# Performance work log

Measured on AMD Instinct MI355X. Metric: run time of the kernel, lower is better.

## Reference

```python
import jax, jax.numpy as jnp
import numpy as np

N = 2_000_000      # total active voxels across the batch (post sparse-conv stack)
C = 128            # channels out of the last SparseConv3d block
B = 256            # batch_size
NUM_CLASSES = 4


def _linear_params(key, fan_in, fan_out):
    kw, kb = jax.random.split(key)
    bound = 1.0 / np.sqrt(fan_in)
    W = jax.random.uniform(kw, (fan_in, fan_out), jnp.float32, -bound, bound)
    b = jax.random.uniform(kb, (fan_out,), jnp.float32, -bound, bound)
    return W, b


def setup_inputs() -> dict:
    key = jax.random.key(0)
    ks = jax.random.split(key, 6)
    features = jax.random.normal(ks[0], (N, C), dtype=jnp.float32)
    batch_ids = jnp.sort(jax.random.randint(ks[1], (N,), 0, B, dtype=jnp.int32))
    W1, b1 = _linear_params(ks[2], 2 * C, 128)
    W2, b2 = _linear_params(ks[3], 128, 64)
    W3, b3 = _linear_params(ks[4], 64, 32)
    W4, b4 = _linear_params(ks[5], 32, NUM_CLASSES)
    return {
        "features": features, "batch_ids": batch_ids, "batch_size": B,
        "W1": W1, "b1": b1, "W2": W2, "b2": b2,
        "W3": W3, "b3": b3, "W4": W4, "b4": b4,
    }


def reference(features, batch_ids, batch_size, W1, b1, W2, b2, W3, b3, W4, b4):
    # Fused segment mean+max pooling (replaces the per-batch Python loop).
    seg_sum = jax.ops.segment_sum(features, batch_ids, num_segments=batch_size,
                                  indices_are_sorted=True)            # [B, C]
    counts = jax.ops.segment_sum(jnp.ones((features.shape[0],), features.dtype),
                                 batch_ids, num_segments=batch_size,
                                 indices_are_sorted=True)             # [B]
    seg_max = jax.ops.segment_max(features, batch_ids, num_segments=batch_size,
                                  indices_are_sorted=True)            # [B, C]
    nonempty = (counts > 0)[:, None]
    seg_mean = jnp.where(nonempty, seg_sum / jnp.maximum(counts, 1.0)[:, None], 0.0)
    seg_max = jnp.where(nonempty, seg_max, 0.0)  # empty segments -> zeros (as in torch code)
    pooled = jnp.concatenate([seg_mean, seg_max], axis=1)             # [B, 2C]
    # fc head (Dropout is identity in eval mode)
    h = jax.nn.relu(pooled @ W1 + b1)
    h = jax.nn.relu(h @ W2 + b2)
    h = jax.nn.relu(h @ W3 + b3)
    return h @ W4 + b4                                                # [B, num_classes]
```

## Files before the change

### kernel.cpp

```cpp
#include <hip/hip_runtime.h>

#define CC 128
#define C4V 32
#define RPB 1024
#define UNR 8

typedef float f4v __attribute__((ext_vector_type(4)));

__device__ __forceinline__ f4v vsplat(float x) {
    f4v r; r.x = x; r.y = x; r.z = x; r.w = x; return r;
}

__device__ __forceinline__ unsigned fkey(float f) {
    unsigned b = __float_as_uint(f);
    return (b & 0x80000000u) ? ~b : (b | 0x80000000u);
}
__device__ __forceinline__ float fdec(unsigned k) {
    unsigned b = (k & 0x80000000u) ? (k & 0x7FFFFFFFu) : ~k;
    return __uint_as_float(b);
}

__device__ __forceinline__ void flush_seg(int seg, int c4, const f4v& sum, const f4v& mx,
                                          int cnt, float* __restrict__ seg_sum,
                                          unsigned* __restrict__ seg_maxk, int* __restrict__ seg_cnt) {
    float* sp = seg_sum + (size_t)seg * CC + c4 * 4;
    atomicAdd(sp + 0, sum.x);
    atomicAdd(sp + 1, sum.y);
    atomicAdd(sp + 2, sum.z);
    atomicAdd(sp + 3, sum.w);
    unsigned* mp = seg_maxk + (size_t)seg * CC + c4 * 4;
    atomicMax(mp + 0, fkey(mx.x));
    atomicMax(mp + 1, fkey(mx.y));
    atomicMax(mp + 2, fkey(mx.z));
    atomicMax(mp + 3, fkey(mx.w));
    if (c4 == 0) atomicAdd(&seg_cnt[seg], cnt);
}

__global__ void __launch_bounds__(256) pool_kernel(
    const float* __restrict__ feats, const int* __restrict__ ids, int N,
    float* __restrict__ seg_sum, unsigned* __restrict__ seg_maxk,
    int* __restrict__ seg_cnt)
{
    __shared__ int sids[RPB];

    const int c4 = threadIdx.x & 31;
    const int rl = threadIdx.x >> 5;
    const long long r0 = (long long)blockIdx.x * RPB;
    const int nrows = (r0 + RPB <= N) ? RPB : (int)(N - r0);

    for (int i = threadIdx.x; i < nrows; i += 256)
        sids[i] = ids[r0 + i];
    __syncthreads();

    f4v sum = vsplat(0.f);
    f4v mx  = vsplat(-3.4e38f);
    int cur = -1, cnt = 0;

    const f4v* __restrict__ fp = (const f4v*)feats + ((long long)r0 + rl) * C4V + c4;

    if (nrows == RPB) {
        #pragma unroll 1
        for (int it = 0; it < RPB / (8 * UNR); ++it) {
            const int lb = it * (8 * UNR) + rl;

            f4v v[UNR];
            #pragma unroll
            for (int k = 0; k < UNR; ++k)
                v[k] = __builtin_nontemporal_load(fp + (size_t)(it * (8 * UNR) + 8 * k) * C4V);

            int idv[UNR];
            #pragma unroll
            for (int k = 0; k < UNR; ++k)
                idv[k] = sids[lb + 8 * k];

            bool same = true;
            #pragma unroll
            for (int k = 0; k < UNR; ++k) same &= (idv[k] == cur);

            if (same) {
                #pragma unroll
                for (int k = 0; k < UNR; ++k) {
                    sum.x += v[k].x; sum.y += v[k].y; sum.z += v[k].z; sum.w += v[k].w;
                    mx.x = fmaxf(mx.x, v[k].x); mx.y = fmaxf(mx.y, v[k].y);
                    mx.z = fmaxf(mx.z, v[k].z); mx.w = fmaxf(mx.w, v[k].w);
                }
                cnt += UNR;
            } else {
                #pragma unroll
                for (int k = 0; k < UNR; ++k) {
                    if (idv[k] != cur) {
                        if (cur >= 0)
                            flush_seg(cur, c4, sum, mx, cnt, seg_sum, seg_maxk, seg_cnt);
                        cur = idv[k];
                        sum = vsplat(0.f);
                        mx  = vsplat(-3.4e38f);
                        cnt = 0;
                    }
                    sum.x += v[k].x; sum.y += v[k].y; sum.z += v[k].z; sum.w += v[k].w;
                    mx.x = fmaxf(mx.x, v[k].x); mx.y = fmaxf(mx.y, v[k].y);
                    mx.z = fmaxf(mx.z, v[k].z); mx.w = fmaxf(mx.w, v[k].w);
                    cnt++;
                }
            }
        }
    } else {
        for (int lr = rl; lr < nrows; lr += 8) {
            int id = sids[lr];
            f4v v = fp[(size_t)(lr - rl) * C4V];
            if (id != cur) {
                if (cur >= 0)
                    flush_seg(cur, c4, sum, mx, cnt, seg_sum, seg_maxk, seg_cnt);
                cur = id;
                sum = vsplat(0.f);
                mx  = vsplat(-3.4e38f);
                cnt = 0;
            }
            sum.x += v.x; sum.y += v.y; sum.z += v.z; sum.w += v.w;
            mx.x = fmaxf(mx.x, v.x); mx.y = fmaxf(mx.y, v.y);
            mx.z = fmaxf(mx.z, v.z); mx.w = fmaxf(mx.w, v.w);
            cnt++;
        }
    }
    if (cur >= 0)
        flush_seg(cur, c4, sum, mx, cnt, seg_sum, seg_maxk, seg_cnt);
}

__global__ void __launch_bounds__(128) head_kernel(
    const float* __restrict__ seg_sum, const unsigned* __restrict__ seg_maxk,
    const int* __restrict__ seg_cnt,
    const float* __restrict__ W1, const float* __restrict__ b1,
    const float* __restrict__ W2, const float* __restrict__ b2,
    const float* __restrict__ W3, const float* __restrict__ b3,
    const float* __restrict__ W4, const float* __restrict__ b4,
    float* __restrict__ out)
{
    __shared__ float pooled[2 * CC];
    __shared__ float h1s[128];
    __shared__ float h2s[64];
    __shared__ float h3s[32];

    const int b = blockIdx.x;
    const int t = threadIdx.x;

    const int cnt = seg_cnt[b];
    const float inv = (cnt > 0) ? (1.f / (float)cnt) : 0.f;

    {
        float s = seg_sum[(size_t)b * CC + t];
        unsigned k = seg_maxk[(size_t)b * CC + t];
        pooled[t] = s * inv;
        pooled[CC + t] = (cnt > 0) ? fdec(k) : 0.f;
    }
    __syncthreads();

    {
        float acc = b1[t];
        for (int i = 0; i < 2 * CC; i++) acc += pooled[i] * W1[i * 128 + t];
        h1s[t] = fmaxf(acc, 0.f);
    }
    __syncthreads();

    if (t < 64) {
        float acc = b2[t];
        for (int i = 0; i < 128; i++) acc += h1s[i] * W2[i * 64 + t];
        h2s[t] = fmaxf(acc, 0.f);
    }
    __syncthreads();

    if (t < 32) {
        float acc = b3[t];
        for (int i = 0; i < 64; i++) acc += h2s[i] * W3[i * 32 + t];
        h3s[t] = fmaxf(acc, 0.f);
    }
    __syncthreads();

    if (t < 4) {
        float acc = b4[t];
        for (int i = 0; i < 32; i++) acc += h3s[i] * W4[i * 4 + t];
        out[b * 4 + t] = acc;
    }
}

extern "C" void kernel_launch(void* const* d_in, const int* in_sizes, int n_in,
                              void* d_out, int out_size, void* d_ws, size_t ws_size,
                              hipStream_t stream) {
    const float* feats = (const float*)d_in[0];
    const int*   ids   = (const int*)d_in[1];
    const float* W1 = (const float*)d_in[3];
    const float* b1 = (const float*)d_in[4];
    const float* W2 = (const float*)d_in[5];
    const float* b2 = (const float*)d_in[6];
    const float* W3 = (const float*)d_in[7];
    const float* b3 = (const float*)d_in[8];
    const float* W4 = (const float*)d_in[9];
    const float* b4 = (const float*)d_in[10];
    float* out = (float*)d_out;

    const int N = in_sizes[1];
    const int NCLS = in_sizes[10];
    const int B = out_size / NCLS;

    float*    seg_sum  = (float*)d_ws;
    unsigned* seg_maxk = (unsigned*)(seg_sum + (size_t)B * CC);
    int*      seg_cnt  = (int*)(seg_maxk + (size_t)B * CC);
    const size_t init_bytes = (size_t)B * CC * 4 * 2 + (size_t)B * 4;
    hipMemsetAsync(d_ws, 0, init_bytes, stream);

    const int grid = (N + RPB - 1) / RPB;
    pool_kernel<<<grid, 256, 0, stream>>>(feats, ids, N, seg_sum, seg_maxk, seg_cnt);
    head_kernel<<<B, 128, 0, stream>>>(seg_sum, seg_maxk, seg_cnt,
                                       W1, b1, W2, b2, W3, b3, W4, b4, out);
}
```

Measured before the change: 1.285 ms.

## Precompute segment boundaries per block and reduce across warps before atomics

```diff
diff --git a/kernel.cpp b/kernel.cpp
--- a/kernel.cpp
+++ b/kernel.cpp
@@ -3,12 +3,18 @@
 #define CC 128
 #define C4V 32
 #define RPB 1024
-#define UNR 8
+#define MAXB 300
 
 typedef float f4v __attribute__((ext_vector_type(4)));
 
 __device__ __forceinline__ f4v vsplat(float x) {
     f4v r; r.x = x; r.y = x; r.z = x; r.w = x; return r;
+}
+__device__ __forceinline__ f4v vmax4(f4v a, f4v b) {
+    f4v r;
+    r.x = fmaxf(a.x, b.x); r.y = fmaxf(a.y, b.y);
+    r.z = fmaxf(a.z, b.z); r.w = fmaxf(a.w, b.w);
+    return r;
 }
 
 __device__ __forceinline__ unsigned fkey(float f) {
@@ -42,68 +48,107 @@
     int* __restrict__ seg_cnt)
 {
     __shared__ int sids[RPB];
-
-    const int c4 = threadIdx.x & 31;
-    const int rl = threadIdx.x >> 5;
+    __shared__ int bpos[MAXB + 1];
+    __shared__ int nb;
+    __shared__ f4v red_s[8][32];
+    __shared__ f4v red_m[8][32];
+
+    const int tid = threadIdx.x;
+    const int c4 = tid & 31;
+    const int rl = tid >> 5;
     const long long r0 = (long long)blockIdx.x * RPB;
-    const int nrows = (r0 + RPB <= N) ? RPB : (int)(N - r0);
-
-    for (int i = threadIdx.x; i < nrows; i += 256)
+    const int nrows = (r0 + RPB <= (long long)N) ? RPB : (int)(N - r0);
+
+    if (tid == 0) nb = 0;
+    for (int i = tid; i < nrows; i += 256)
         sids[i] = ids[r0 + i];
     __syncthreads();
 
-    f4v sum = vsplat(0.f);
-    f4v mx  = vsplat(-3.4e38f);
-    int cur = -1, cnt = 0;
-
-    const f4v* __restrict__ fp = (const f4v*)feats + ((long long)r0 + rl) * C4V + c4;
-
-    if (nrows == RPB) {
-        #pragma unroll 1
-        for (int it = 0; it < RPB / (8 * UNR); ++it) {
-            const int lb = it * (8 * UNR) + rl;
-
-            f4v v[UNR];
-            #pragma unroll
-            for (int k = 0; k < UNR; ++k)
-                v[k] = __builtin_nontemporal_load(fp + (size_t)(it * (8 * UNR) + 8 * k) * C4V);
-
-            int idv[UNR];
-            #pragma unroll
-            for (int k = 0; k < UNR; ++k)
-                idv[k] = sids[lb + 8 * k];
-
-            bool same = true;
-            #pragma unroll
-            for (int k = 0; k < UNR; ++k) same &= (idv[k] == cur);
-
-            if (same) {
+    for (int i = tid; i < nrows; i += 256) {
+        if (i == 0 || sids[i] != sids[i - 1]) {
+            int k = atomicAdd(&nb, 1);
+            if (k < MAXB) bpos[k] = i;
+        }
+    }
+    __syncthreads();
+    const int NB = nb;
+
+    if (NB <= MAXB) {
+        if (tid == 0) {
+            for (int a = 1; a < NB; ++a) {
+                int v = bpos[a]; int b = a - 1;
+                while (b >= 0 && bpos[b] > v) { bpos[b + 1] = bpos[b]; --b; }
+                bpos[b + 1] = v;
+            }
+            bpos[NB] = nrows;
+        }
+        __syncthreads();
+
+        const f4v* fbase = (const f4v*)feats + (size_t)r0 * C4V + c4;
+
+        for (int s = 0; s < NB; ++s) {
+            const int lo  = bpos[s];
+            const int hi  = bpos[s + 1];
+            const int seg = sids[lo];
+            const int len = hi - lo;
+
+            f4v sum = vsplat(0.f);
+            f4v mx  = vsplat(-3.4e38f);
+            const f4v* p = fbase + (size_t)lo * C4V;
+
+            int j = rl;
+            for (; j + 56 < len; j += 64) {
+                f4v v[8];
                 #pragma unroll
-                for (int k = 0; k < UNR; ++k) {
-                    sum.x += v[k].x; sum.y += v[k].y; sum.z += v[k].z; sum.w += v[k].w;
-                    mx.x = fmaxf(mx.x, v[k].x); mx.y = fmaxf(mx.y, v[k].y);
-                    mx.z = fmaxf(mx.z, v[k].z); mx.w = fmaxf(mx.w, v[k].w);
+                for (int k = 0; k < 8; ++k)
+                    v[k] = p[(size_t)(j + 8 * k) * C4V];
+                #pragma unroll
+                for (int k = 0; k < 8; ++k) {
+                    sum += v[k];
+                    mx = vmax4(mx, v[k]);
                 }
-                cnt += UNR;
-            } else {
-                #pragma unroll
-                for (int k = 0; k < UNR; ++k) {
-                    if (idv[k] != cur) {
-                        if (cur >= 0)
-                            flush_seg(cur, c4, sum, mx, cnt, seg_sum, seg_maxk, seg_cnt);
-                        cur = idv[k];
-                        sum = vsplat(0.f);
-                        mx  = vsplat(-3.4e38f);
-                        cnt = 0;
-                    }
-                    sum.x += v[k].x; sum.y += v[k].y; sum.z += v[k].z; sum.w += v[k].w;
-                    mx.x = fmaxf(mx.x, v[k].x); mx.y = fmaxf(mx.y, v[k].y);
-                    mx.z = fmaxf(mx.z, v[k].z); mx.w = fmaxf(mx.w, v[k].w);
-                    cnt++;
-                }
-            }
+            }
+            for (; j < len; j += 8) {
+                f4v v = p[(size_t)j * C4V];
+                sum += v;
+                mx = vmax4(mx, v);
+            }
+
+            red_s[rl][c4] = sum;
+            red_m[rl][c4] = mx;
+            __syncthreads();
+            if (rl < 4) {
+                red_s[rl][c4] += red_s[rl + 4][c4];
+                red_m[rl][c4] = vmax4(red_m[rl][c4], red_m[rl + 4][c4]);
+            }
+            __syncthreads();
+            if (rl < 2) {
+                red_s[rl][c4] += red_s[rl + 2][c4];
+                red_m[rl][c4] = vmax4(red_m[rl][c4], red_m[rl + 2][c4]);
+            }
+            __syncthreads();
+            if (rl == 0) {
+                f4v fs = red_s[0][c4] + red_s[1][c4];
+                f4v fm = vmax4(red_m[0][c4], red_m[1][c4]);
+                float* sp = seg_sum + (size_t)seg * CC + c4 * 4;
+                atomicAdd(sp + 0, fs.x);
+                atomicAdd(sp + 1, fs.y);
+                atomicAdd(sp + 2, fs.z);
+                atomicAdd(sp + 3, fs.w);
+                unsigned* mp = seg_maxk + (size_t)seg * CC + c4 * 4;
+                atomicMax(mp + 0, fkey(fm.x));
+                atomicMax(mp + 1, fkey(fm.y));
+                atomicMax(mp + 2, fkey(fm.z));
+                atomicMax(mp + 3, fkey(fm.w));
+                if (c4 == 0) atomicAdd(&seg_cnt[seg], len);
+            }
+            __syncthreads();
         }
     } else {
+        f4v sum = vsplat(0.f);
+        f4v mx  = vsplat(-3.4e38f);
+        int cur = -1, cnt = 0;
+        const f4v* fp = (const f4v*)feats + ((size_t)r0 + rl) * C4V + c4;
         for (int lr = rl; lr < nrows; lr += 8) {
             int id = sids[lr];
             f4v v = fp[(size_t)(lr - rl) * C4V];
@@ -115,14 +160,13 @@
                 mx  = vsplat(-3.4e38f);
                 cnt = 0;
             }
-            sum.x += v.x; sum.y += v.y; sum.z += v.z; sum.w += v.w;
-            mx.x = fmaxf(mx.x, v.x); mx.y = fmaxf(mx.y, v.y);
-            mx.z = fmaxf(mx.z, v.z); mx.w = fmaxf(mx.w, v.w);
+            sum += v;
+            mx = vmax4(mx, v);
             cnt++;
         }
-    }
-    if (cur >= 0)
-        flush_seg(cur, c4, sum, mx, cnt, seg_sum, seg_maxk, seg_cnt);
+        if (cur >= 0)
+            flush_seg(cur, c4, sum, mx, cnt, seg_sum, seg_maxk, seg_cnt);
+    }
 }
 
 __global__ void __launch_bounds__(128) head_kernel(
```

Result: no change. 1.304 ms (+1.5%).
